# Kernel tuning notes

Measured on AMD Instinct MI355X. Metric: run time of the kernel, lower is better.

## Reference

```python
import jax, jax.numpy as jnp
import numpy as np

WIDTH = [256, 512, 256]
NUM = 5       # grid intervals -> NUM+1 grid points per edge
K = 3         # spline order
BATCH = 256
GRID_RANGE = (-1.0, 1.0)


def extend_grid(grid, k):
    # grid: (size, NUM+1) -> (size, NUM+1+2k); mirrors pykan B_batch extend
    h = (grid[:, -1:] - grid[:, :1]) / (grid.shape[1] - 1)
    for _ in range(k):
        grid = jnp.concatenate([grid[:, :1] - h, grid, grid[:, -1:] + h], axis=1)
    return grid


def b_batch(x, grid, k):
    # Cox-de Boor B-spline bases. x: (size, B); grid: (size, G) extended.
    # returns (size, G-k-1, B)
    xg = x[:, None, :]
    g = grid[:, :, None]
    B = ((xg >= g[:, :-1]) & (xg < g[:, 1:])).astype(x.dtype)
    for d in range(1, k + 1):
        left = (xg - g[:, : -(d + 1)]) / (g[:, d:-1] - g[:, : -(d + 1)])
        right = (g[:, d + 1:] - xg) / (g[:, d + 1:] - g[:, 1:-d])
        B = left * B[:, :-1] + right * B[:, 1:]
    return B


def kan_layer(x, grid, coef, scale_base, scale_sp, bias, in_dim, out_dim):
    # x: (B, in_dim); edge ordering is (out, in) flattened, matching
    # torch einsum('ij,k->ikj', x, ones(out)).reshape(B, size)
    Bn = x.shape[0]
    size = out_dim * in_dim
    xe = jnp.broadcast_to(x[:, None, :], (Bn, out_dim, in_dim)).reshape(Bn, size)
    basis = b_batch(xe.T, extend_grid(grid, K), K)        # (size, NUM+K, B)
    spl = jnp.einsum('sn,snb->bs', coef, basis)            # (B, size)
    y = scale_base[None, :] * jax.nn.silu(xe) + scale_sp[None, :] * spl
    postacts = y.reshape(Bn, out_dim, in_dim)
    x_out = postacts.sum(-1) + bias                        # bias: (1, out_dim)
    # per-edge grid stats, as in KAN.forward
    gr = grid.reshape(out_dim, in_dim, -1)
    input_range = gr[:, :, -1] - gr[:, :, 0] + 1e-4
    acts_scale = jnp.mean(jnp.abs(postacts), axis=0) / input_range
    acts_std = jnp.std(postacts, axis=0, ddof=1)           # torch.std is unbiased
    return x_out, acts_scale, acts_std


def _make_params(key):
    params = {}
    for l in range(len(WIDTH) - 1):
        i, o = WIDTH[l], WIDTH[l + 1]
        size = i * o
        k1, k2, key = jax.random.split(key, 3)
        params[f'grid{l}'] = jnp.broadcast_to(
            jnp.linspace(GRID_RANGE[0], GRID_RANGE[1], NUM + 1, dtype=jnp.float32),
            (size, NUM + 1)) + jnp.zeros((size, NUM + 1), dtype=jnp.float32)
        params[f'coef{l}'] = jax.random.normal(k1, (size, NUM + K), dtype=jnp.float32) * 0.1
        params[f'scale_base{l}'] = (1.0 / np.sqrt(i)).astype(np.float32) + \
            (jax.random.normal(k2, (size,), dtype=jnp.float32) * 2.0 - 1.0) * 0.1
        params[f'scale_sp{l}'] = jnp.ones((size,), dtype=jnp.float32)
        params[f'bias{l}'] = jnp.zeros((1, o), dtype=jnp.float32)
    return params


def setup_inputs() -> dict:
    key = jax.random.key(0)
    kx, kp = jax.random.split(key)
    inp = {'x': jax.random.normal(kx, (BATCH, WIDTH[0]), dtype=jnp.float32)}
    inp.update(_make_params(kp))
    return inp


def reference(x, grid0, coef0, scale_base0, scale_sp0, bias0,
              grid1, coef1, scale_base1, scale_sp1, bias1):
    x, sc0, st0 = kan_layer(x, grid0, coef0, scale_base0, scale_sp0, bias0, WIDTH[0], WIDTH[1])
    x, sc1, st1 = kan_layer(x, grid1, coef1, scale_base1, scale_sp1, bias1, WIDTH[1], WIDTH[2])
    return x, sc0, st0, sc1, st1
```

## Files before the change

### kernel.cpp

```cpp
#include <hip/hip_runtime.h>
#include <math.h>

constexpr int BATCH = 256;

typedef short short8 __attribute__((ext_vector_type(8)));
typedef float f32x4 __attribute__((ext_vector_type(4)));

__device__ __forceinline__ unsigned short f2bf(float f) {
    unsigned int u = __float_as_uint(f);
    u += 0x7FFFu + ((u >> 16) & 1u);
    return (unsigned short)(u >> 16);
}
__device__ __forceinline__ unsigned int pack2(float a, float b) {
    return (unsigned int)f2bf(a) | ((unsigned int)f2bf(b) << 16);
}

__device__ __forceinline__ void basis_eval(
    float x, const float* __restrict__ grid, int ii, float out[9])
{
    float g[6];
#pragma unroll
    for (int k = 0; k < 6; ++k) g[k] = grid[(size_t)ii * 6 + k];
    float h = (g[5] - g[0]) * 0.2f;

    float t[12];
    t[0] = g[0] - 3.f * h; t[1] = g[0] - 2.f * h; t[2] = g[0] - h;
#pragma unroll
    for (int k = 0; k < 6; ++k) t[3 + k] = g[k];
    t[9] = g[5] + h; t[10] = g[5] + 2.f * h; t[11] = g[5] + 3.f * h;

    float Bv[11];
#pragma unroll
    for (int j = 0; j < 11; ++j)
        Bv[j] = (x >= t[j] && x < t[j + 1]) ? 1.0f : 0.0f;

#pragma unroll
    for (int d = 1; d <= 3; ++d) {
#pragma unroll
        for (int j = 0; j + d < 11; ++j) {
            float left  = __fdividef(x - t[j],         t[j + d] - t[j]);
            float right = __fdividef(t[j + d + 1] - x, t[j + d + 1] - t[j + 1]);
            Bv[j] = left * Bv[j] + right * Bv[j + 1];
        }
    }

#pragma unroll
    for (int k = 0; k < 8; ++k) out[k] = Bv[k];
    out[8] = __fdividef(x, 1.0f + __expf(-x));
}

__device__ __forceinline__ void store_rec12(unsigned short* rec, const float v[9])
{
    uint2* p = (uint2*)rec;
    p[0] = make_uint2(pack2(v[0], v[1]), pack2(v[2], v[3]));
    p[1] = make_uint2(pack2(v[4], v[5]), pack2(v[6], v[7]));
    p[2] = make_uint2(pack2(v[8], 0.f), 0u);
}

__device__ __forceinline__ void store_rec32(unsigned short* rec, const float v[9])
{
    uint4* p = (uint4*)rec;
    p[0] = make_uint4(pack2(v[0], v[1]), pack2(v[2], v[3]),
                      pack2(v[4], v[5]), pack2(v[6], v[7]));
    p[1] = make_uint4(pack2(v[8], 0.f), 0u, 0u, 0u);
    p[2] = make_uint4(0u, 0u, 0u, 0u);
    p[3] = make_uint4(0u, 0u, 0u, 0u);
}

__device__ __forceinline__ void merge_body(
    const float* __restrict__ coef, const float* __restrict__ ssp,
    const float* __restrict__ sb, unsigned short* __restrict__ wc9,
    unsigned short* __restrict__ wc32, int s)
{
    float sspv = ssp[s], sbv = sb[s];
    const float4* c = (const float4*)(coef + (size_t)s * 8);
    float4 c0 = c[0], c1 = c[1];
    float v[9] = { sspv * c0.x, sspv * c0.y, sspv * c0.z, sspv * c0.w,
                   sspv * c1.x, sspv * c1.y, sspv * c1.z, sspv * c1.w, sbv };
    store_rec12(wc9 + (size_t)s * 12, v);
    store_rec32(wc32 + (size_t)s * 32, v);
}

__device__ __forceinline__ void gemm0_fused(
    const unsigned short* __restrict__ wc9_0, const unsigned short* __restrict__ bas9_0,
    const float* __restrict__ bias0, const float* __restrict__ grid1,
    unsigned short* __restrict__ bas9_1, unsigned short* __restrict__ bas32_1,
    int bid, float (*T)[16][17])
{
    constexpr int K2 = 3072, KW = K2 / 4;
    int mt = bid >> 4, nt = bid & 15;
    int t = threadIdx.x, l = t & 63, w = t >> 6;
    int m0 = mt * 16;
    int n0 = nt * 16;

    const unsigned short* pa = wc9_0  + (size_t)(m0 + (l & 15)) * K2 + w * KW + ((l >> 4) * 8);
    const unsigned short* pb = bas9_0 + (size_t)(n0 + (l & 15)) * K2 + w * KW + ((l >> 4) * 8);

    f32x4 acc = {0.f, 0.f, 0.f, 0.f};
#pragma unroll 8
    for (int kk = 0; kk < KW / 32; ++kk) {
        short8 av = *(const short8*)pa; pa += 32;
        short8 bv = *(const short8*)pb; pb += 32;
        acc = __builtin_amdgcn_mfma_f32_16x16x32_bf16(av, bv, acc, 0, 0, 0);
    }

#pragma unroll
    for (int r = 0; r < 4; ++r)
        T[w][(l >> 4) * 4 + r][l & 15] = acc[r];
    __syncthreads();

    int ii_loc = t & 15, b_loc = t >> 4;
    float d = T[0][ii_loc][b_loc] + T[1][ii_loc][b_loc]
            + T[2][ii_loc][b_loc] + T[3][ii_loc][b_loc];
    int ii = m0 + ii_loc;
    float xv = d + bias0[ii];
    float out[9];
    basis_eval(xv, grid1, ii, out);
    size_t p = (size_t)(n0 + b_loc) * 512 + ii;
    store_rec12(bas9_1 + p * 12, out);
    store_rec32(bas32_1 + p * 32, out);
    __syncthreads();
}

__device__ __forceinline__ void gemm1_fused(
    const unsigned short* __restrict__ bas9_1, const unsigned short* __restrict__ wc9_1,
    const float* __restrict__ bias1, float* __restrict__ x2, int bid, float (*T)[16][17])
{
    constexpr int K2 = 6144, KW = K2 / 4;
    int mt = bid >> 4, nt = bid & 15;
    int t = threadIdx.x, l = t & 63, w = t >> 6;
    int m0 = mt * 16;
    int n0 = nt * 16;

    const unsigned short* pa = bas9_1 + (size_t)(m0 + (l & 15)) * K2 + w * KW + ((l >> 4) * 8);
    const unsigned short* pb = wc9_1  + (size_t)(n0 + (l & 15)) * K2 + w * KW + ((l >> 4) * 8);

    f32x4 acc = {0.f, 0.f, 0.f, 0.f};
#pragma unroll 8
    for (int kk = 0; kk < KW / 32; ++kk) {
        short8 av = *(const short8*)pa; pa += 32;
        short8 bv = *(const short8*)pb; pb += 32;
        acc = __builtin_amdgcn_mfma_f32_16x16x32_bf16(av, bv, acc, 0, 0, 0);
    }

#pragma unroll
    for (int r = 0; r < 4; ++r)
        T[w][(l >> 4) * 4 + r][l & 15] = acc[r];
    __syncthreads();

    int o_loc = t & 15, b_loc = t >> 4;
    float d = T[0][b_loc][o_loc] + T[1][b_loc][o_loc]
            + T[2][b_loc][o_loc] + T[3][b_loc][o_loc];
    int o = n0 + o_loc;
    x2[(size_t)(m0 + b_loc) * 256 + o] = d + bias1[o];
}

template <int I>
__device__ __forceinline__ void stats_mfma(
    const unsigned short* __restrict__ bas32, const unsigned short* __restrict__ wc32,
    const float* __restrict__ grid, float* __restrict__ sc, float* __restrict__ st,
    int id)
{
    int og = id / I, ii = id % I;
    int l = threadIdx.x & 63;
    int row = l & 15, chunk = l >> 4;

    short8 bfrag[4];
#pragma unroll
    for (int q = 0; q < 4; ++q) {
        int o = og * 64 + q * 16 + row;
        bfrag[q] = *(const short8*)(wc32 + ((size_t)o * I + ii) * 32 + chunk * 8);
    }

    float ab[4], sm[4], sq[4];
#pragma unroll
    for (int q = 0; q < 4; ++q) { ab[q] = 0.f; sm[q] = 0.f; sq[q] = 0.f; }

    for (int bt = 0; bt < 16; ++bt) {
        int b = bt * 16 + row;
        short8 av = *(const short8*)(bas32 + ((size_t)b * I + ii) * 32 + chunk * 8);
#pragma unroll
        for (int q = 0; q < 4; ++q) {
            f32x4 d = {0.f, 0.f, 0.f, 0.f};
            d = __builtin_amdgcn_mfma_f32_16x16x32_bf16(av, bfrag[q], d, 0, 0, 0);
#pragma unroll
            for (int r = 0; r < 4; ++r) {
                float y = d[r];
                ab[q] += fabsf(y);
                sm[q] += y;
                sq[q] = fmaf(y, y, sq[q]);
            }
        }
    }

#pragma unroll
    for (int q = 0; q < 4; ++q) {
        ab[q] += __shfl_xor(ab[q], 16); ab[q] += __shfl_xor(ab[q], 32);
        sm[q] += __shfl_xor(sm[q], 16); sm[q] += __shfl_xor(sm[q], 32);
        sq[q] += __shfl_xor(sq[q], 16); sq[q] += __shfl_xor(sq[q], 32);
    }

    if (l < 16) {
#pragma unroll
        for (int q = 0; q < 4; ++q) {
            int o = og * 64 + q * 16 + l;
            size_t s = (size_t)o * I + ii;
            float range = grid[s * 6 + 5] - grid[s * 6] + 1e-4f;
            sc[s] = (ab[q] * (1.0f / BATCH)) / range;
            float var = (sq[q] - sm[q] * sm[q] * (1.0f / BATCH)) * (1.0f / (BATCH - 1));
            st[s] = sqrtf(fmaxf(var, 0.0f));
        }
    }
}

__global__ __launch_bounds__(256) void k1_prep(
    const float* __restrict__ coef0, const float* __restrict__ ssp0,
    const float* __restrict__ sb0,   unsigned short* __restrict__ wc9_0,
    unsigned short* __restrict__ wc32_0,
    const float* __restrict__ coef1, const float* __restrict__ ssp1,
    const float* __restrict__ sb1,   unsigned short* __restrict__ wc9_1,
    unsigned short* __restrict__ wc32_1,
    const float* __restrict__ x, const float* __restrict__ grid0,
    unsigned short* __restrict__ bas9_0, unsigned short* __restrict__ bas32_0)
{
    int bid = blockIdx.x, t = threadIdx.x;
    if (bid < 512)  { merge_body(coef0, ssp0, sb0, wc9_0, wc32_0, bid * 256 + t); return; }
    if (bid < 1024) { merge_body(coef1, ssp1, sb1, wc9_1, wc32_1, (bid - 512) * 256 + t); return; }
    int tile = bid - 1024;
    int bt = tile >> 4, it = tile & 15;
    int ii = it * 16 + (t & 15), b = bt * 16 + (t >> 4);
    float out[9];
    basis_eval(x[(size_t)b * 256 + ii], grid0, ii, out);
    size_t p = (size_t)b * 256 + ii;
    store_rec12(bas9_0 + p * 12, out);
    store_rec32(bas32_0 + p * 32, out);
}

__global__ __launch_bounds__(256) void k2_sweep0(
    const unsigned short* __restrict__ wc9_0, const unsigned short* __restrict__ bas9_0,
    const float* __restrict__ bias0, const float* __restrict__ grid1,
    unsigned short* __restrict__ bas9_1, unsigned short* __restrict__ bas32_1,
    const unsigned short* __restrict__ bas32_0, const unsigned short* __restrict__ wc32_0,
    const float* __restrict__ grid0, float* __restrict__ sc0, float* __restrict__ st0)
{
    __shared__ float Tsh[4][16][17];
    int bid = blockIdx.x;
    if (bid < 512) {
        gemm0_fused(wc9_0, bas9_0, bias0, grid1, bas9_1, bas32_1, bid, Tsh);
    } else {
        int id = (bid - 512) * 4 + (threadIdx.x >> 6);
        stats_mfma<256>(bas32_0, wc32_0, grid0, sc0, st0, id);
    }
}

__global__ __launch_bounds__(256) void k3_sweep1(
    const unsigned short* __restrict__ bas9_1, const unsigned short* __restrict__ wc9_1,
    const float* __restrict__ bias1, float* __restrict__ x2,
    const unsigned short* __restrict__ bas32_1, const unsigned short* __restrict__ wc32_1,
    const float* __restrict__ grid1, float* __restrict__ sc1, float* __restrict__ st1)
{
    __shared__ float Tsh[4][16][17];
    int bid = blockIdx.x;
    if (bid < 256) {
        gemm1_fused(bas9_1, wc9_1, bias1, x2, bid, Tsh);
    } else {
        int id = (bid - 256) * 4 + (threadIdx.x >> 6);
        stats_mfma<512>(bas32_1, wc32_1, grid1, sc1, st1, id);
    }
}

extern "C" void kernel_launch(void* const* d_in, const int* in_sizes, int n_in,
                              void* d_out, int out_size, void* d_ws, size_t ws_size,
                              hipStream_t stream)
{
    const float* x     = (const float*)d_in[0];
    const float* grid0 = (const float*)d_in[1];
    const float* coef0 = (const float*)d_in[2];
    const float* sb0   = (const float*)d_in[3];
    const float* ssp0  = (const float*)d_in[4];
    const float* bias0 = (const float*)d_in[5];
    const float* grid1 = (const float*)d_in[6];
    const float* coef1 = (const float*)d_in[7];
    const float* sb1   = (const float*)d_in[8];
    const float* ssp1  = (const float*)d_in[9];
    const float* bias1 = (const float*)d_in[10];

    float* out = (float*)d_out;
    float* x2  = out;
    float* sc0 = out + 65536;
    float* st0 = out + 196608;
    float* sc1 = out + 327680;
    float* st1 = out + 458752;

    char* w = (char*)d_ws;
    unsigned short* wc9_0   = (unsigned short*)w; w += (size_t)512 * 3072 * 2;
    unsigned short* wc9_1   = (unsigned short*)w; w += (size_t)256 * 6144 * 2;
    unsigned short* bas9_0  = (unsigned short*)w; w += (size_t)256 * 3072 * 2;
    unsigned short* bas9_1  = (unsigned short*)w; w += (size_t)256 * 6144 * 2;
    unsigned short* wc32_0  = (unsigned short*)w; w += (size_t)131072 * 32 * 2;
    unsigned short* wc32_1  = (unsigned short*)w; w += (size_t)131072 * 32 * 2;
    unsigned short* bas32_0 = (unsigned short*)w; w += (size_t)65536 * 32 * 2;
    unsigned short* bas32_1 = (unsigned short*)w; w += (size_t)131072 * 32 * 2;

    k1_prep<<<1280, 256, 0, stream>>>(
        coef0, ssp0, sb0, wc9_0, wc32_0,
        coef1, ssp1, sb1, wc9_1, wc32_1,
        x, grid0, bas9_0, bas32_0);

    k2_sweep0<<<1024, 256, 0, stream>>>(
        wc9_0, bas9_0, bias0, grid1, bas9_1, bas32_1,
        bas32_0, wc32_0, grid0, sc0, st0);

    k3_sweep1<<<768, 256, 0, stream>>>(
        bas9_1, wc9_1, bias1, x2,
        bas32_1, wc32_1, grid1, sc1, st1);
}
```

Measured before the change: 63.40 us.

## Unify bf16 records to 16-wide layout and use 32x32 MFMA for stats

Replaces the separate 12-element GEMM records and 32-element stats records with a single 16-element bf16 record per edge, used by both the GEMMs and the stats pass. The stats pass switches from four 16x16x32 MFMAs per batch tile to one 32x32x16 MFMA covering 32 outputs, so its grid grows. This removes duplicate writes of padded records and reduces workspace traffic. In exchange, the GEMM K dimension grows from 12 to 16 per edge, adding zero-padded reads, and the stats launch now has more blocks.

```diff
diff --git a/kernel.cpp b/kernel.cpp
--- a/kernel.cpp
+++ b/kernel.cpp
@@ -5,6 +5,7 @@
 
 typedef short short8 __attribute__((ext_vector_type(8)));
 typedef float f32x4 __attribute__((ext_vector_type(4)));
+typedef float f32x16 __attribute__((ext_vector_type(16)));
 
 __device__ __forceinline__ unsigned short f2bf(float f) {
     unsigned int u = __float_as_uint(f);
@@ -49,52 +50,39 @@
     out[8] = __fdividef(x, 1.0f + __expf(-x));
 }
 
-__device__ __forceinline__ void store_rec12(unsigned short* rec, const float v[9])
-{
-    uint2* p = (uint2*)rec;
-    p[0] = make_uint2(pack2(v[0], v[1]), pack2(v[2], v[3]));
-    p[1] = make_uint2(pack2(v[4], v[5]), pack2(v[6], v[7]));
-    p[2] = make_uint2(pack2(v[8], 0.f), 0u);
-}
-
-__device__ __forceinline__ void store_rec32(unsigned short* rec, const float v[9])
+__device__ __forceinline__ void store_rec16(unsigned short* rec, const float v[9])
 {
     uint4* p = (uint4*)rec;
     p[0] = make_uint4(pack2(v[0], v[1]), pack2(v[2], v[3]),
                       pack2(v[4], v[5]), pack2(v[6], v[7]));
     p[1] = make_uint4(pack2(v[8], 0.f), 0u, 0u, 0u);
-    p[2] = make_uint4(0u, 0u, 0u, 0u);
-    p[3] = make_uint4(0u, 0u, 0u, 0u);
 }
 
 __device__ __forceinline__ void merge_body(
     const float* __restrict__ coef, const float* __restrict__ ssp,
-    const float* __restrict__ sb, unsigned short* __restrict__ wc9,
-    unsigned short* __restrict__ wc32, int s)
+    const float* __restrict__ sb, unsigned short* __restrict__ wc16, int s)
 {
     float sspv = ssp[s], sbv = sb[s];
     const float4* c = (const float4*)(coef + (size_t)s * 8);
     float4 c0 = c[0], c1 = c[1];
     float v[9] = { sspv * c0.x, sspv * c0.y, sspv * c0.z, sspv * c0.w,
                    sspv * c1.x, sspv * c1.y, sspv * c1.z, sspv * c1.w, sbv };
-    store_rec12(wc9 + (size_t)s * 12, v);
-    store_rec32(wc32 + (size_t)s * 32, v);
+    store_rec16(wc16 + (size_t)s * 16, v);
 }
 
 __device__ __forceinline__ void gemm0_fused(
-    const unsigned short* __restrict__ wc9_0, const unsigned short* __restrict__ bas9_0,
+    const unsigned short* __restrict__ wc16_0, const unsigned short* __restrict__ bas16_0,
     const float* __restrict__ bias0, const float* __restrict__ grid1,
-    unsigned short* __restrict__ bas9_1, unsigned short* __restrict__ bas32_1,
-    int bid, float (*T)[16][17])
-{
-    constexpr int K2 = 3072, KW = K2 / 4;
+    unsigned short* __restrict__ bas16_1, int bid, float (*T)[16][17])
+{
+    constexpr int K2 = 256 * 16, KW = K2 / 4;
     int mt = bid >> 4, nt = bid & 15;
     int t = threadIdx.x, l = t & 63, w = t >> 6;
     int m0 = mt * 16;
     int n0 = nt * 16;
 
-    const unsigned short* pa = wc9_0  + (size_t)(m0 + (l & 15)) * K2 + w * KW + ((l >> 4) * 8);
-    const unsigned short* pb = bas9_0 + (size_t)(n0 + (l & 15)) * K2 + w * KW + ((l >> 4) * 8);
+    const unsigned short* pa = wc16_0  + (size_t)(m0 + (l & 15)) * K2 + w * KW + ((l >> 4) * 8);
+    const unsigned short* pb = bas16_0 + (size_t)(n0 + (l & 15)) * K2 + w * KW + ((l >> 4) * 8);
 
     f32x4 acc = {0.f, 0.f, 0.f, 0.f};
 #pragma unroll 8
@@ -116,24 +104,22 @@
     float xv = d + bias0[ii];
     float out[9];
     basis_eval(xv, grid1, ii, out);
-    size_t p = (size_t)(n0 + b_loc) * 512 + ii;
-    store_rec12(bas9_1 + p * 12, out);
-    store_rec32(bas32_1 + p * 32, out);
+    store_rec16(bas16_1 + ((size_t)(n0 + b_loc) * 512 + ii) * 16, out);
     __syncthreads();
 }
 
 __device__ __forceinline__ void gemm1_fused(
-    const unsigned short* __restrict__ bas9_1, const unsigned short* __restrict__ wc9_1,
+    const unsigned short* __restrict__ bas16_1, const unsigned short* __restrict__ wc16_1,
     const float* __restrict__ bias1, float* __restrict__ x2, int bid, float (*T)[16][17])
 {
-    constexpr int K2 = 6144, KW = K2 / 4;
+    constexpr int K2 = 512 * 16, KW = K2 / 4;
     int mt = bid >> 4, nt = bid & 15;
     int t = threadIdx.x, l = t & 63, w = t >> 6;
     int m0 = mt * 16;
     int n0 = nt * 16;
 
-    const unsigned short* pa = bas9_1 + (size_t)(m0 + (l & 15)) * K2 + w * KW + ((l >> 4) * 8);
-    const unsigned short* pb = wc9_1  + (size_t)(n0 + (l & 15)) * K2 + w * KW + ((l >> 4) * 8);
+    const unsigned short* pa = bas16_1 + (size_t)(m0 + (l & 15)) * K2 + w * KW + ((l >> 4) * 8);
+    const unsigned short* pb = wc16_1  + (size_t)(n0 + (l & 15)) * K2 + w * KW + ((l >> 4) * 8);
 
     f32x4 acc = {0.f, 0.f, 0.f, 0.f};
 #pragma unroll 8
@@ -157,115 +143,96 @@
 
 template <int I>
 __device__ __forceinline__ void stats_mfma(
-    const unsigned short* __restrict__ bas32, const unsigned short* __restrict__ wc32,
+    const unsigned short* __restrict__ bas16, const unsigned short* __restrict__ wc16,
     const float* __restrict__ grid, float* __restrict__ sc, float* __restrict__ st,
     int id)
 {
     int og = id / I, ii = id % I;
     int l = threadIdx.x & 63;
-    int row = l & 15, chunk = l >> 4;
-
-    short8 bfrag[4];
-#pragma unroll
-    for (int q = 0; q < 4; ++q) {
-        int o = og * 64 + q * 16 + row;
-        bfrag[q] = *(const short8*)(wc32 + ((size_t)o * I + ii) * 32 + chunk * 8);
-    }
-
-    float ab[4], sm[4], sq[4];
-#pragma unroll
-    for (int q = 0; q < 4; ++q) { ab[q] = 0.f; sm[q] = 0.f; sq[q] = 0.f; }
-
-    for (int bt = 0; bt < 16; ++bt) {
-        int b = bt * 16 + row;
-        short8 av = *(const short8*)(bas32 + ((size_t)b * I + ii) * 32 + chunk * 8);
-#pragma unroll
-        for (int q = 0; q < 4; ++q) {
-            f32x4 d = {0.f, 0.f, 0.f, 0.f};
-            d = __builtin_amdgcn_mfma_f32_16x16x32_bf16(av, bfrag[q], d, 0, 0, 0);
-#pragma unroll
-            for (int r = 0; r < 4; ++r) {
-                float y = d[r];
-                ab[q] += fabsf(y);
-                sm[q] += y;
-                sq[q] = fmaf(y, y, sq[q]);
-            }
+    int row = l & 31, chunk = l >> 5;
+
+    short8 bfrag = *(const short8*)(
+        wc16 + ((size_t)(og * 32 + row) * I + ii) * 16 + chunk * 8);
+
+    float ab = 0.f, sm = 0.f, sq = 0.f;
+    for (int bt = 0; bt < BATCH / 32; ++bt) {
+        int b = bt * 32 + row;
+        short8 av = *(const short8*)(
+            bas16 + ((size_t)b * I + ii) * 16 + chunk * 8);
+        f32x16 d;
+#pragma unroll
+        for (int r = 0; r < 16; ++r) d[r] = 0.f;
+        d = __builtin_amdgcn_mfma_f32_32x32x16_bf16(av, bfrag, d, 0, 0, 0);
+#pragma unroll
+        for (int r = 0; r < 16; ++r) {
+            float y = d[r];
+            ab += fabsf(y);
+            sm += y;
+            sq = fmaf(y, y, sq);
         }
     }
 
-#pragma unroll
-    for (int q = 0; q < 4; ++q) {
-        ab[q] += __shfl_xor(ab[q], 16); ab[q] += __shfl_xor(ab[q], 32);
-        sm[q] += __shfl_xor(sm[q], 16); sm[q] += __shfl_xor(sm[q], 32);
-        sq[q] += __shfl_xor(sq[q], 16); sq[q] += __shfl_xor(sq[q], 32);
-    }
-
-    if (l < 16) {
-#pragma unroll
-        for (int q = 0; q < 4; ++q) {
-            int o = og * 64 + q * 16 + l;
-            size_t s = (size_t)o * I + ii;
-            float range = grid[s * 6 + 5] - grid[s * 6] + 1e-4f;
-            sc[s] = (ab[q] * (1.0f / BATCH)) / range;
-            float var = (sq[q] - sm[q] * sm[q] * (1.0f / BATCH)) * (1.0f / (BATCH - 1));
-            st[s] = sqrtf(fmaxf(var, 0.0f));
-        }
+    ab += __shfl_xor(ab, 32);
+    sm += __shfl_xor(sm, 32);
+    sq += __shfl_xor(sq, 32);
+
+    if (l < 32) {
+        int o = og * 32 + l;
+        size_t s = (size_t)o * I + ii;
+        float range = grid[s * 6 + 5] - grid[s * 6] + 1e-4f;
+        sc[s] = (ab * (1.0f / BATCH)) / range;
+        float var = (sq - sm * sm * (1.0f / BATCH)) * (1.0f / (BATCH - 1));
+        st[s] = sqrtf(fmaxf(var, 0.0f));
     }
 }
 
 __global__ __launch_bounds__(256) void k1_prep(
     const float* __restrict__ coef0, const float* __restrict__ ssp0,
-    const float* __restrict__ sb0,   unsigned short* __restrict__ wc9_0,
-    unsigned short* __restrict__ wc32_0,
+    const float* __restrict__ sb0,   unsigned short* __restrict__ wc16_0,
     const float* __restrict__ coef1, const float* __restrict__ ssp1,
-    const float* __restrict__ sb1,   unsigned short* __restrict__ wc9_1,
-    unsigned short* __restrict__ wc32_1,
+    const float* __restrict__ sb1,   unsigned short* __restrict__ wc16_1,
     const float* __restrict__ x, const float* __restrict__ grid0,
-    unsigned short* __restrict__ bas9_0, unsigned short* __restrict__ bas32_0)
+    unsigned short* __restrict__ bas16_0)
 {
     int bid = blockIdx.x, t = threadIdx.x;
-    if (bid < 512)  { merge_body(coef0, ssp0, sb0, wc9_0, wc32_0, bid * 256 + t); return; }
-    if (bid < 1024) { merge_body(coef1, ssp1, sb1, wc9_1, wc32_1, (bid - 512) * 256 + t); return; }
+    if (bid < 512)  { merge_body(coef0, ssp0, sb0, wc16_0, bid * 256 + t); return; }
+    if (bid < 1024) { merge_body(coef1, ssp1, sb1, wc16_1, (bid - 512) * 256 + t); return; }
     int tile = bid - 1024;
     int bt = tile >> 4, it = tile & 15;
     int ii = it * 16 + (t & 15), b = bt * 16 + (t >> 4);
     float out[9];
     basis_eval(x[(size_t)b * 256 + ii], grid0, ii, out);
-    size_t p = (size_t)b * 256 + ii;
-    store_rec12(bas9_0 + p * 12, out);
-    store_rec32(bas32_0 + p * 32, out);
+    store_rec16(bas16_0 + ((size_t)b * 256 + ii) * 16, out);
 }
 
 __global__ __launch_bounds__(256) void k2_sweep0(
-    const unsigned short* __restrict__ wc9_0, const unsigned short* __restrict__ bas9_0,
+    const unsigned short* __restrict__ wc16_0, const unsigned short* __restrict__ bas16_0,
     const float* __restrict__ bias0, const float* __restrict__ grid1,
-    unsigned short* __restrict__ bas9_1, unsigned short* __restrict__ bas32_1,
-    const unsigned short* __restrict__ bas32_0, const unsigned short* __restrict__ wc32_0,
+    unsigned short* __restrict__ bas16_1,
     const float* __restrict__ grid0, float* __restrict__ sc0, float* __restrict__ st0)
 {
     __shared__ float Tsh[4][16][17];
     int bid = blockIdx.x;
     if (bid < 512) {
-        gemm0_fused(wc9_0, bas9_0, bias0, grid1, bas9_1, bas32_1, bid, Tsh);
+        gemm0_fused(wc16_0, bas16_0, bias0, grid1, bas16_1, bid, Tsh);
     } else {
         int id = (bid - 512) * 4 + (threadIdx.x >> 6);
-        stats_mfma<256>(bas32_0, wc32_0, grid0, sc0, st0, id);
+        stats_mfma<256>(bas16_0, wc16_0, grid0, sc0, st0, id);
     }
 }
 
 __global__ __launch_bounds__(256) void k3_sweep1(
-    const unsigned short* __restrict__ bas9_1, const unsigned short* __restrict__ wc9_1,
+    const unsigned short* __restrict__ bas16_1, const unsigned short* __restrict__ wc16_1,
     const float* __restrict__ bias1, float* __restrict__ x2,
-    const unsigned short* __restrict__ bas32_1, const unsigned short* __restrict__ wc32_1,
     const float* __restrict__ grid1, float* __restrict__ sc1, float* __restrict__ st1)
 {
     __shared__ float Tsh[4][16][17];
     int bid = blockIdx.x;
     if (bid < 256) {
-        gemm1_fused(bas9_1, wc9_1, bias1, x2, bid, Tsh);
+        gemm1_fused(bas16_1, wc16_1, bias1, x2, bid, Tsh);
     } else {
         int id = (bid - 256) * 4 + (threadIdx.x >> 6);
-        stats_mfma<512>(bas32_1, wc32_1, grid1, sc1, st1, id);
+        stats_mfma<512>(bas16_1, wc16_1, grid1, sc1, st1, id);
     }
 }
 
@@ -293,25 +260,19 @@
     float* st1 = out + 458752;
 
     char* w = (char*)d_ws;
-    unsigned short* wc9_0   = (unsigned short*)w; w += (size_t)512 * 3072 * 2;
-    unsigned short* wc9_1   = (unsigned short*)w; w += (size_t)256 * 6144 * 2;
-    unsigned short* bas9_0  = (unsigned short*)w; w += (size_t)256 * 3072 * 2;
-    unsigned short* bas9_1  = (unsigned short*)w; w += (size_t)256 * 6144 * 2;
-    unsigned short* wc32_0  = (unsigned short*)w; w += (size_t)131072 * 32 * 2;
-    unsigned short* wc32_1  = (unsigned short*)w; w += (size_t)131072 * 32 * 2;
-    unsigned short* bas32_0 = (unsigned short*)w; w += (size_t)65536 * 32 * 2;
-    unsigned short* bas32_1 = (unsigned short*)w; w += (size_t)131072 * 32 * 2;
+    unsigned short* wc16_0  = (unsigned short*)w; w += (size_t)131072 * 32;
+    unsigned short* wc16_1  = (unsigned short*)w; w += (size_t)131072 * 32;
+    unsigned short* bas16_0 = (unsigned short*)w; w += (size_t)65536 * 32;
+    unsigned short* bas16_1 = (unsigned short*)w; w += (size_t)131072 * 32;
 
     k1_prep<<<1280, 256, 0, stream>>>(
-        coef0, ssp0, sb0, wc9_0, wc32_0,
-        coef1, ssp1, sb1, wc9_1, wc32_1,
-        x, grid0, bas9_0, bas32_0);
-
-    k2_sweep0<<<1024, 256, 0, stream>>>(
-        wc9_0, bas9_0, bias0, grid1, bas9_1, bas32_1,
-        bas32_0, wc32_0, grid0, sc0, st0);
-
-    k3_sweep1<<<768, 256, 0, stream>>>(
-        bas9_1, wc9_1, bias1, x2,
-        bas32_1, wc32_1, grid1, sc1, st1);
-}
+        coef0, ssp0, sb0, wc16_0,
+        coef1, ssp1, sb1, wc16_1,
+        x, grid0, bas16_0);
+
+    k2_sweep0<<<1536, 256, 0, stream>>>(
+        wc16_0, bas16_0, bias0, grid1, bas16_1, grid0, sc0, st0);
+
+    k3_sweep1<<<1280, 256, 0, stream>>>(
+        bas16_1, wc16_1, bias1, x2, grid1, sc1, st1);
+}
```

New measurement: 57.10 us. 1.11x faster.
